# Optimization experiments

Hardware: AMD Instinct MI355X
Metric: run time of the kernel (lower is better)

Reference implementation:

```python
import jax, jax.numpy as jnp
import numpy as np

HEADS = 4
DIM_HEAD = 32
SCALE = DIM_HEAD ** -0.5


def setup_inputs() -> dict:
    key = jax.random.key(0)
    k1, k2, k3 = jax.random.split(key, 3)
    dim = 256
    hidden = HEADS * DIM_HEAD  # 128
    x = jax.random.normal(k1, (2, dim, 64, 64), dtype=jnp.float32)
    # Conv2d 1x1 weights flattened to [out_ch, in_ch]
    w_qkv = jax.random.normal(k2, (hidden * 3, dim), dtype=jnp.float32) * (dim ** -0.5)
    w_out = jax.random.normal(k3, (dim, hidden), dtype=jnp.float32) * (hidden ** -0.5)
    b_out = jnp.zeros((dim,), dtype=jnp.float32)
    return {"x": x, "w_qkv": w_qkv, "w_out": w_out, "b_out": b_out}


def reference(x, w_qkv, w_out, b_out):
    b, c, h, w = x.shape
    n = h * w
    # 1x1 conv == channel matmul: [b, 3*hidden, h, w]
    qkv = jnp.einsum('bchw,oc->bohw', x, w_qkv)
    q, k, v = jnp.split(qkv, 3, axis=1)
    # 'b (heads d) x y -> b heads d (x y)'
    def to_heads(t):
        return t.reshape(b, HEADS, DIM_HEAD, n)
    q, k, v = to_heads(q), to_heads(k), to_heads(v)
    q = q * SCALE
    dots = jnp.einsum('bhdi,bhdj->bhij', q, k)  # [b, heads, n, n]
    dots = dots - jax.lax.stop_gradient(jnp.max(dots, axis=-1, keepdims=True))
    attn = jax.nn.softmax(dots, axis=-1)
    out = jnp.einsum('bhij,bhdj->bhid', attn, v)  # [b, heads, n, d]
    # 'b heads (x y) d -> b (heads d) x y'
    out = out.transpose(0, 1, 3, 2).reshape(b, HEADS * DIM_HEAD, h, w)
    return jnp.einsum('bchw,oc->bohw', out, w_out) + b_out[None, :, None, None]
```

## Files before the change

kernel.cpp:

```cpp
#include <hip/hip_runtime.h>
#include <hip/hip_bf16.h>
#include <math.h>

#define NB 2
#define CIN 256
#define NPOS 4096
#define HID 128
#define NHEAD 4
#define DHEAD 32
#define NBH 8
#define NSPLIT 4
#define QSCALE 0.2550348676144781f

typedef __bf16 bf16;
typedef __attribute__((ext_vector_type(8))) __bf16 bf16x8;
typedef __attribute__((ext_vector_type(4))) __bf16 bf16x4;
typedef __attribute__((ext_vector_type(4))) float f32x4;

union B8 { bf16x8 v; bf16x4 h[2]; };

#define XT_OFF  0u
#define QB_OFF  4194304u
#define KB_OFF  6291456u
#define VT_OFF  8388608u
#define AOP_OFF 10485760u
#define LP_OFF  18874368u
#define WB_OFF  19398656u
#define WOB_OFF 19595264u

__global__ __launch_bounds__(256) void prep_kernel(const float* __restrict__ x,
                                                   const float* __restrict__ wqkv,
                                                   const float* __restrict__ wout,
                                                   bf16* __restrict__ xt,
                                                   bf16* __restrict__ wb,
                                                   bf16* __restrict__ wob) {
    const int t = threadIdx.x;
    if (blockIdx.y == 4) {
        int tid = blockIdx.x * 256 + t;
        if (blockIdx.z == 0) {
            #pragma unroll
            for (int u = 0; u < 6; ++u) {
                int idx = tid * 6 + u;
                float v = wqkv[idx];
                if (idx < 32768) v *= QSCALE;
                wb[idx] = (bf16)v;
            }
        } else {
            wob[tid * 2]     = (bf16)wout[tid * 2];
            wob[tid * 2 + 1] = (bf16)wout[tid * 2 + 1];
        }
        return;
    }
    const int b  = blockIdx.z;
    const int c0 = blockIdx.y * 64;
    const int i0 = blockIdx.x * 64;
    __shared__ float Ts[64][65];
    const float* xb = x + (size_t)b * CIN * NPOS;
    #pragma unroll
    for (int u = 0; u < 4; ++u) {
        int c = (t >> 4) + u * 16;
        int i = (t & 15) * 4;
        float4 v = *(const float4*)(xb + (size_t)(c0 + c) * NPOS + i0 + i);
        Ts[c][i] = v.x; Ts[c][i + 1] = v.y; Ts[c][i + 2] = v.z; Ts[c][i + 3] = v.w;
    }
    __syncthreads();
    int i  = t & 63;
    int cc = (t >> 6) * 16;
    B8 o0, o1;
    #pragma unroll
    for (int j = 0; j < 8; ++j) {
        o0.v[j] = (bf16)Ts[cc + j][i];
        o1.v[j] = (bf16)Ts[cc + 8 + j][i];
    }
    bf16* dst = xt + ((size_t)b * NPOS + i0 + i) * CIN + c0 + cc;
    *(bf16x8*)dst       = o0.v;
    *(bf16x8*)(dst + 8) = o1.v;
}

__global__ __launch_bounds__(256) void qkv_kernel(const bf16* __restrict__ xt,
                                                  const bf16* __restrict__ wb,
                                                  bf16* __restrict__ qb,
                                                  bf16* __restrict__ kb,
                                                  bf16* __restrict__ vtb) {
    const int i0 = blockIdx.x * 64;
    const int ot = blockIdx.y * 64;
    const int b  = blockIdx.z;
    const int t  = threadIdx.x;
    const int w  = t >> 6;
    const int lane = t & 63;
    const int quad = lane >> 4;
    const int li   = lane & 15;

    __shared__ bf16 Bs[64][36];

    f32x4 acc[4];
    #pragma unroll
    for (int n = 0; n < 4; ++n) acc[n] = (f32x4){0.f, 0.f, 0.f, 0.f};

    const bf16* xrow = xt + ((size_t)b * NPOS + i0) * CIN;
    const int si = t >> 2;
    const int sk = (t & 3) * 8;

    for (int k0 = 0; k0 < CIN; k0 += 32) {
        __syncthreads();
        B8 g0;
        g0.v = *(const bf16x8*)(xrow + (size_t)si * CIN + k0 + sk);
        *(bf16x4*)&Bs[si][sk]     = g0.h[0];
        *(bf16x4*)&Bs[si][sk + 4] = g0.h[1];
        __syncthreads();
        bf16x8 afrag = *(const bf16x8*)(wb + (size_t)(ot + w * 16 + li) * CIN + k0 + quad * 8);
        #pragma unroll
        for (int n = 0; n < 4; ++n) {
            B8 bf;
            bf.h[0] = *(const bf16x4*)&Bs[n * 16 + li][quad * 8];
            bf.h[1] = *(const bf16x4*)&Bs[n * 16 + li][quad * 8 + 4];
            acc[n] = __builtin_amdgcn_mfma_f32_16x16x32_bf16(afrag, bf.v, acc[n], 0, 0, 0);
        }
    }

    const int obase = ot + w * 16;
    const int sect  = obase >> 7;
    const int oo    = obase & 127;
    const int h     = oo >> 5;
    const int dbase = (oo & 31) + quad * 4;
    const int bh    = b * NHEAD + h;

    #pragma unroll
    for (int n = 0; n < 4; ++n) {
        int i = i0 + n * 16 + li;
        f32x4 v = acc[n];
        if (sect <= 1) {
            bf16x4 pk;
            #pragma unroll
            for (int r = 0; r < 4; ++r) pk[r] = (bf16)v[r];
            bf16* base = (sect == 0) ? qb : kb;
            *(bf16x4*)(base + ((size_t)bh * NPOS + i) * DHEAD + dbase) = pk;
        } else {
            #pragma unroll
            for (int r = 0; r < 4; ++r)
                vtb[((size_t)bh * DHEAD + dbase + r) * NPOS + i] = (bf16)v[r];
        }
    }
}

__global__ __launch_bounds__(256, 4) void fattn_kernel(const bf16* __restrict__ qb,
                                                       const bf16* __restrict__ kb,
                                                       const bf16* __restrict__ vtb,
                                                       bf16* __restrict__ aop,
                                                       float* __restrict__ lpart) {
    const int id    = blockIdx.x;
    const int g     = id & 31;
    const int iblk  = id >> 5;
    const int bh    = g >> 2;
    const int split = g & 3;
    const int w     = threadIdx.x >> 6;
    const int lane  = threadIdx.x & 63;
    const int quad  = lane >> 4;
    const int li    = lane & 15;
    const int i0    = iblk * 128 + w * 32;
    const int j_lo  = split * 1024;

    const bf16* qrow = qb + (size_t)bh * NPOS * DHEAD;
    const bf16x8 qf0 = *(const bf16x8*)(qrow + (size_t)(i0 + li) * DHEAD + quad * 8);
    const bf16x8 qf1 = *(const bf16x8*)(qrow + (size_t)(i0 + 16 + li) * DHEAD + quad * 8);
    const bf16* kbase  = kb  + (size_t)bh * NPOS * DHEAD;
    const bf16* vtbase = vtb + (size_t)bh * DHEAD * NPOS;

    bf16x8 ones;
    #pragma unroll
    for (int j = 0; j < 8; ++j) ones[j] = (bf16)1.0f;

    f32x4 o00 = {0.f,0.f,0.f,0.f}, o01 = {0.f,0.f,0.f,0.f};
    f32x4 o10 = {0.f,0.f,0.f,0.f}, o11 = {0.f,0.f,0.f,0.f};
    f32x4 l0  = {0.f,0.f,0.f,0.f}, l1  = {0.f,0.f,0.f,0.f};

    __shared__ alignas(16) bf16 Kbuf[2][64][32];
    __shared__ alignas(16) bf16 Vbuf[2][32][64];
    __shared__ alignas(16) bf16 plds[4][32][68];

    const f32x4 zero = {0.f,0.f,0.f,0.f};

    const int krow = w * 16 + (lane >> 2);
    const int kcol = (lane & 3) * 8;
    const int vrow = w * 8 + (lane >> 3);
    const int vchk = lane & 7;
    const int vslot = vchk ^ (vrow & 7);
    const bf16* ksrc = kbase + (size_t)krow * DHEAD + kcol;
    const bf16* vsrc = vtbase + (size_t)vrow * NPOS + vchk * 8;

    bf16x8 kg, vg;

    kg = *(const bf16x8*)(ksrc + (size_t)j_lo * DHEAD);
    vg = *(const bf16x8*)(vsrc + j_lo);
    *(bf16x8*)&Kbuf[0][krow][kcol]      = kg;
    *(bf16x8*)&Vbuf[0][vrow][vslot * 8] = vg;
    __syncthreads();

    for (int it = 0; it < 16; ++it) {
        const int cur = it & 1;
        const int j0  = j_lo + it * 64;
        if (it < 15) {
            kg = *(const bf16x8*)(ksrc + (size_t)(j0 + 64) * DHEAD);
            vg = *(const bf16x8*)(vsrc + j0 + 64);
        }
        bf16x8 kf[4];
        #pragma unroll
        for (int tt = 0; tt < 4; ++tt)
            kf[tt] = *(const bf16x8*)&Kbuf[cur][16 * tt + li][quad * 8];
        f32x4 s0[4], s1[4];
        #pragma unroll
        for (int tt = 0; tt < 4; ++tt) {
            s0[tt] = __builtin_amdgcn_mfma_f32_16x16x32_bf16(kf[tt], qf0, zero, 0, 0, 0);
            s1[tt] = __builtin_amdgcn_mfma_f32_16x16x32_bf16(kf[tt], qf1, zero, 0, 0, 0);
        }
        #pragma unroll
        for (int tt = 0; tt < 4; ++tt) {
            bf16x4 p0, p1;
            #pragma unroll
            for (int r = 0; r < 4; ++r) {
                p0[r] = (bf16)__builtin_amdgcn_exp2f(s0[tt][r]);
                p1[r] = (bf16)__builtin_amdgcn_exp2f(s1[tt][r]);
            }
            *(bf16x4*)&plds[w][li][16 * tt + quad * 4]      = p0;
            *(bf16x4*)&plds[w][16 + li][16 * tt + quad * 4] = p1;
        }
        #pragma unroll
        for (int h2 = 0; h2 < 2; ++h2) {
            B8 pf0, pf1;
            pf0.h[0] = *(const bf16x4*)&plds[w][li][h2 * 32 + quad * 8];
            pf0.h[1] = *(const bf16x4*)&plds[w][li][h2 * 32 + quad * 8 + 4];
            pf1.h[0] = *(const bf16x4*)&plds[w][16 + li][h2 * 32 + quad * 8];
            pf1.h[1] = *(const bf16x4*)&plds[w][16 + li][h2 * 32 + quad * 8 + 4];
            const int s0s = (h2 * 4 + quad) ^ (li & 7);
            bf16x8 v0f = *(const bf16x8*)&Vbuf[cur][li][s0s * 8];
            bf16x8 v1f = *(const bf16x8*)&Vbuf[cur][16 + li][s0s * 8];
            l0  = __builtin_amdgcn_mfma_f32_16x16x32_bf16(ones, pf0.v, l0,  0, 0, 0);
            l1  = __builtin_amdgcn_mfma_f32_16x16x32_bf16(ones, pf1.v, l1,  0, 0, 0);
            o00 = __builtin_amdgcn_mfma_f32_16x16x32_bf16(v0f,  pf0.v, o00, 0, 0, 0);
            o01 = __builtin_amdgcn_mfma_f32_16x16x32_bf16(v1f,  pf0.v, o01, 0, 0, 0);
            o10 = __builtin_amdgcn_mfma_f32_16x16x32_bf16(v0f,  pf1.v, o10, 0, 0, 0);
            o11 = __builtin_amdgcn_mfma_f32_16x16x32_bf16(v1f,  pf1.v, o11, 0, 0, 0);
        }
        if (it < 15) {
            *(bf16x8*)&Kbuf[cur ^ 1][krow][kcol]      = kg;
            *(bf16x8*)&Vbuf[cur ^ 1][vrow][vslot * 8] = vg;
        }
        __syncthreads();
    }

    const int b = bh >> 2, h = bh & 3;
    {
        const int i = i0 + li;
        bf16* dst = aop + (((size_t)(split * NB + b) * NPOS + i) * HID) + h * DHEAD;
        bf16x4 pk0, pk1;
        #pragma unroll
        for (int r = 0; r < 4; ++r) { pk0[r] = (bf16)o00[r]; pk1[r] = (bf16)o01[r]; }
        *(bf16x4*)(dst + quad * 4)      = pk0;
        *(bf16x4*)(dst + 16 + quad * 4) = pk1;
        if (quad == 0) lpart[((size_t)split * NBH + bh) * NPOS + i] = l0[0];
    }
    {
        const int i = i0 + 16 + li;
        bf16* dst = aop + (((size_t)(split * NB + b) * NPOS + i) * HID) + h * DHEAD;
        bf16x4 pk0, pk1;
        #pragma unroll
        for (int r = 0; r < 4; ++r) { pk0[r] = (bf16)o10[r]; pk1[r] = (bf16)o11[r]; }
        *(bf16x4*)(dst + quad * 4)      = pk0;
        *(bf16x4*)(dst + 16 + quad * 4) = pk1;
        if (quad == 0) lpart[((size_t)split * NBH + bh) * NPOS + i] = l1[0];
    }
}

__global__ __launch_bounds__(256) void proj_kernel(const bf16* __restrict__ aop,
                                                   const float* __restrict__ lpart,
                                                   const bf16* __restrict__ wob,
                                                   const float* __restrict__ bout,
                                                   float* __restrict__ y) {
    const int i0 = blockIdx.x * 16;
    const int b  = blockIdx.y;
    const int t  = threadIdx.x;
    const int w  = t >> 6;
    const int lane = t & 63;
    const int quad = lane >> 4;
    const int li   = lane & 15;

    __shared__ bf16 Bs[16][132];

    {
        const int row = t >> 4;
        const int cp  = (t & 15) * 8;
        const int gi  = i0 + row;
        const int h   = cp >> 5;

        float lsum = 0.f;
        #pragma unroll
        for (int s = 0; s < NSPLIT; ++s)
            lsum += lpart[((size_t)s * NBH + b * NHEAD + h) * NPOS + gi];
        const float invl = __builtin_amdgcn_rcpf(lsum);

        float vals[8];
        #pragma unroll
        for (int j = 0; j < 8; ++j) vals[j] = 0.f;
        #pragma unroll
        for (int s = 0; s < NSPLIT; ++s) {
            bf16x8 u = *(const bf16x8*)(aop + (((size_t)(s * NB + b) * NPOS + gi) * HID) + cp);
            #pragma unroll
            for (int j = 0; j < 8; ++j) vals[j] += (float)u[j];
        }
        B8 pk;
        #pragma unroll
        for (int j = 0; j < 8; ++j) pk.v[j] = (bf16)(vals[j] * invl);
        *(bf16x4*)&Bs[row][cp]     = pk.h[0];
        *(bf16x4*)&Bs[row][cp + 4] = pk.h[1];
    }
    __syncthreads();

    f32x4 acc[4];
    #pragma unroll
    for (int m = 0; m < 4; ++m) acc[m] = (f32x4){0.f, 0.f, 0.f, 0.f};

    #pragma unroll
    for (int k0 = 0; k0 < HID; k0 += 32) {
        B8 bf;
        bf.h[0] = *(const bf16x4*)&Bs[li][k0 + quad * 8];
        bf.h[1] = *(const bf16x4*)&Bs[li][k0 + quad * 8 + 4];
        #pragma unroll
        for (int m = 0; m < 4; ++m) {
            bf16x8 afrag = *(const bf16x8*)(wob + (size_t)(w * 64 + m * 16 + li) * HID + k0 + quad * 8);
            acc[m] = __builtin_amdgcn_mfma_f32_16x16x32_bf16(afrag, bf.v, acc[m], 0, 0, 0);
        }
    }

    float* yb = y + (size_t)b * CIN * NPOS;
    #pragma unroll
    for (int m = 0; m < 4; ++m) {
        const int oc = w * 64 + m * 16 + quad * 4;
        #pragma unroll
        for (int r = 0; r < 4; ++r)
            yb[(size_t)(oc + r) * NPOS + i0 + li] = acc[m][r] + bout[oc + r];
    }
}

extern "C" void kernel_launch(void* const* d_in, const int* in_sizes, int n_in,
                              void* d_out, int out_size, void* d_ws, size_t ws_size,
                              hipStream_t stream) {
    const float* x    = (const float*)d_in[0];
    const float* wqkv = (const float*)d_in[1];
    const float* wout = (const float*)d_in[2];
    const float* bout = (const float*)d_in[3];
    float* y = (float*)d_out;
    char* ws = (char*)d_ws;

    bf16*  xt  = (bf16*)(ws + XT_OFF);
    bf16*  qb  = (bf16*)(ws + QB_OFF);
    bf16*  kb  = (bf16*)(ws + KB_OFF);
    bf16*  vtb = (bf16*)(ws + VT_OFF);
    bf16*  aop = (bf16*)(ws + AOP_OFF);
    float* lp  = (float*)(ws + LP_OFF);
    bf16*  wb  = (bf16*)(ws + WB_OFF);
    bf16*  wob = (bf16*)(ws + WOB_OFF);

    prep_kernel<<<dim3(64, 5, 2), 256, 0, stream>>>(x, wqkv, wout, xt, wb, wob);
    qkv_kernel<<<dim3(64, 6, 2), 256, 0, stream>>>(xt, wb, qb, kb, vtb);
    fattn_kernel<<<dim3(1024), 256, 0, stream>>>(qb, kb, vtb, aop, lp);
    proj_kernel<<<dim3(256, 2), 256, 0, stream>>>(aop, lp, wob, bout, y);
}
```

Before: 107.9 us.

## Keep softmax probabilities in registers by permuting V column layout

The QKV projection now stores V transposed with a permuted position order, so the MFMA output layout of P matches the B-operand layout needed by the PV MFMA. The P tile therefore no longer round-trips through shared memory (the plds buffer is removed), which saves LDS writes and reads per iteration and frees LDS. In exchange, the layouts of two kernels are coupled, and the permuted write pattern in the projection kernel must be exactly consistent for correctness.

```diff
diff --git a/kernel.cpp b/kernel.cpp
--- a/kernel.cpp
+++ b/kernel.cpp
@@ -136,9 +136,10 @@
             bf16* base = (sect == 0) ? qb : kb;
             *(bf16x4*)(base + ((size_t)bh * NPOS + i) * DHEAD + dbase) = pk;
         } else {
+            const int ip = i0 + ((n >> 1) << 5) + ((li >> 2) << 3) + ((n & 1) << 2) + (li & 3);
             #pragma unroll
             for (int r = 0; r < 4; ++r)
-                vtb[((size_t)bh * DHEAD + dbase + r) * NPOS + i] = (bf16)v[r];
+                vtb[((size_t)bh * DHEAD + dbase + r) * NPOS + ip] = (bf16)v[r];
         }
     }
 }
@@ -176,7 +177,6 @@
 
     __shared__ alignas(16) bf16 Kbuf[2][64][32];
     __shared__ alignas(16) bf16 Vbuf[2][32][64];
-    __shared__ alignas(16) bf16 plds[4][32][68];
 
     const f32x4 zero = {0.f,0.f,0.f,0.f};
 
@@ -214,32 +214,24 @@
             s1[tt] = __builtin_amdgcn_mfma_f32_16x16x32_bf16(kf[tt], qf1, zero, 0, 0, 0);
         }
         #pragma unroll
-        for (int tt = 0; tt < 4; ++tt) {
-            bf16x4 p0, p1;
+        for (int h2 = 0; h2 < 2; ++h2) {
+            B8 pa0, pa1;
             #pragma unroll
             for (int r = 0; r < 4; ++r) {
-                p0[r] = (bf16)__builtin_amdgcn_exp2f(s0[tt][r]);
-                p1[r] = (bf16)__builtin_amdgcn_exp2f(s1[tt][r]);
+                pa0.v[r]     = (bf16)__builtin_amdgcn_exp2f(s0[2 * h2][r]);
+                pa0.v[4 + r] = (bf16)__builtin_amdgcn_exp2f(s0[2 * h2 + 1][r]);
+                pa1.v[r]     = (bf16)__builtin_amdgcn_exp2f(s1[2 * h2][r]);
+                pa1.v[4 + r] = (bf16)__builtin_amdgcn_exp2f(s1[2 * h2 + 1][r]);
             }
-            *(bf16x4*)&plds[w][li][16 * tt + quad * 4]      = p0;
-            *(bf16x4*)&plds[w][16 + li][16 * tt + quad * 4] = p1;
-        }
-        #pragma unroll
-        for (int h2 = 0; h2 < 2; ++h2) {
-            B8 pf0, pf1;
-            pf0.h[0] = *(const bf16x4*)&plds[w][li][h2 * 32 + quad * 8];
-            pf0.h[1] = *(const bf16x4*)&plds[w][li][h2 * 32 + quad * 8 + 4];
-            pf1.h[0] = *(const bf16x4*)&plds[w][16 + li][h2 * 32 + quad * 8];
-            pf1.h[1] = *(const bf16x4*)&plds[w][16 + li][h2 * 32 + quad * 8 + 4];
             const int s0s = (h2 * 4 + quad) ^ (li & 7);
             bf16x8 v0f = *(const bf16x8*)&Vbuf[cur][li][s0s * 8];
             bf16x8 v1f = *(const bf16x8*)&Vbuf[cur][16 + li][s0s * 8];
-            l0  = __builtin_amdgcn_mfma_f32_16x16x32_bf16(ones, pf0.v, l0,  0, 0, 0);
-            l1  = __builtin_amdgcn_mfma_f32_16x16x32_bf16(ones, pf1.v, l1,  0, 0, 0);
-            o00 = __builtin_amdgcn_mfma_f32_16x16x32_bf16(v0f,  pf0.v, o00, 0, 0, 0);
-            o01 = __builtin_amdgcn_mfma_f32_16x16x32_bf16(v1f,  pf0.v, o01, 0, 0, 0);
-            o10 = __builtin_amdgcn_mfma_f32_16x16x32_bf16(v0f,  pf1.v, o10, 0, 0, 0);
-            o11 = __builtin_amdgcn_mfma_f32_16x16x32_bf16(v1f,  pf1.v, o11, 0, 0, 0);
+            l0  = __builtin_amdgcn_mfma_f32_16x16x32_bf16(ones, pa0.v, l0,  0, 0, 0);
+            l1  = __builtin_amdgcn_mfma_f32_16x16x32_bf16(ones, pa1.v, l1,  0, 0, 0);
+            o00 = __builtin_amdgcn_mfma_f32_16x16x32_bf16(v0f,  pa0.v, o00, 0, 0, 0);
+            o01 = __builtin_amdgcn_mfma_f32_16x16x32_bf16(v1f,  pa0.v, o01, 0, 0, 0);
+            o10 = __builtin_amdgcn_mfma_f32_16x16x32_bf16(v0f,  pa1.v, o10, 0, 0, 0);
+            o11 = __builtin_amdgcn_mfma_f32_16x16x32_bf16(v1f,  pa1.v, o11, 0, 0, 0);
         }
         if (it < 15) {
             *(bf16x8*)&Kbuf[cur ^ 1][krow][kcol]      = kg;
```

Result: faster. 102.9 us (median of 2 runs) (-4.6%).
